# Performance work log

Measured on AMD Instinct MI355X. Metric: run time of the kernel, lower is better.

Reference implementation:

```python
import jax, jax.numpy as jnp
import numpy as np

N_HEAD = 16


def setup_inputs() -> dict:
    key = jax.random.key(0)
    ks = jax.random.split(key, 6)
    B, T, C = 2, 2048, 1024
    x = jax.random.normal(ks[0], (B, T, C), dtype=jnp.float32)
    mask = jnp.ones((B, T), dtype=jnp.int32)
    s = 1.0 / np.sqrt(C)
    Wqkv = jax.random.normal(ks[1], (C, 3 * C), dtype=jnp.float32) * s
    bqkv = jax.random.normal(ks[2], (3 * C,), dtype=jnp.float32) * 0.02
    Wproj = jax.random.normal(ks[3], (C, C), dtype=jnp.float32) * s
    bproj = jax.random.normal(ks[4], (C,), dtype=jnp.float32) * 0.02
    return {"x": x, "mask": mask, "Wqkv": Wqkv, "bqkv": bqkv,
            "Wproj": Wproj, "bproj": bproj}


def reference(x, mask, Wqkv, bqkv, Wproj, bproj):
    B, T, C = x.shape
    H = N_HEAD
    Dh = C // H
    scale = 1.0 / np.sqrt(Dh)
    qkv = x @ Wqkv + bqkv                       # [B,T,3C]
    q, k, v = jnp.split(qkv, 3, axis=-1)
    # [B,T,C] -> [B,H,T,Dh]
    q = q.reshape(B, T, H, Dh).transpose(0, 2, 1, 3)
    k = k.reshape(B, T, H, Dh).transpose(0, 2, 1, 3)
    v = v.reshape(B, T, H, Dh).transpose(0, 2, 1, 3)
    attn = jnp.einsum('bhid,bhjd->bhij', q, k) * scale  # [B,H,T,T]
    m = mask[:, None, None, :]                  # b j -> b 1 1 j
    attn = jnp.where(m == 0, -jnp.inf, attn)
    attn = jax.nn.softmax(attn, axis=-1)
    y = jnp.einsum('bhij,bhjd->bhid', attn, v)  # [B,H,T,Dh]
    y = y.transpose(0, 2, 1, 3).reshape(B, T, C)
    return y @ Wproj + bproj
```

## Files before the change

### kernel.cpp

```cpp
#include <hip/hip_runtime.h>

using US   = unsigned short;
using bf8  = __attribute__((ext_vector_type(8))) __bf16;
using us8  = __attribute__((ext_vector_type(8))) US;
using us4  = __attribute__((ext_vector_type(4))) US;
using f4   = __attribute__((ext_vector_type(4))) float;
using f8   = __attribute__((ext_vector_type(8))) float;
using f16v = __attribute__((ext_vector_type(16))) float;
using i4   = __attribute__((ext_vector_type(4))) int;
using u2   = __attribute__((ext_vector_type(2))) unsigned;

__device__ __forceinline__ US f2bf(float x) {
  union { float f; unsigned u; } v; v.f = x;
  unsigned r = v.u + 0x7fffu + ((v.u >> 16) & 1u);
  return (US)(r >> 16);
}
__device__ __forceinline__ unsigned cvtpk(float a, float b) {
  unsigned r;
  asm("v_cvt_pk_bf16_f32 %0, %1, %2" : "=v"(r) : "v"(a), "v"(b));
  return r;
}
#if __has_builtin(__builtin_amdgcn_exp2f)
__device__ __forceinline__ float ex2(float x) { return __builtin_amdgcn_exp2f(x); }
#else
__device__ __forceinline__ float ex2(float x) {
  float r;
  asm("v_exp_f32 %0, %1" : "=v"(r) : "v"(x));
  return r;
}
#endif
__device__ __forceinline__ void gl16(const US* g, US* l) {
  __builtin_amdgcn_global_load_lds((const __attribute__((address_space(1))) void*)g,
                                   (__attribute__((address_space(3))) void*)l, 16, 0, 0);
}

__global__ void prep_k(const float* __restrict__ x, US* __restrict__ xb,
                       const float* __restrict__ Wqkv, US* __restrict__ WqkvT,
                       const float* __restrict__ Wproj, US* __restrict__ WprojT) {
  __shared__ float tile[32][33];
  int bid = blockIdx.x;
  if (bid < 2048) {
    int i = bid * 256 + threadIdx.x;
    f8 v = ((const f8*)x)[i];
    us8 o;
#pragma unroll
    for (int j = 0; j < 8; ++j) o[j] = f2bf(v[j]);
    ((us8*)xb)[i] = o;
    return;
  }
  const float* in;
  US* out;
  int R, C, tx0, ty0;
  if (bid < 2048 + 3072) {
    int tid = bid - 2048;
    in = Wqkv; out = WqkvT; R = 1024; C = 3072;
    tx0 = (tid % 96) * 32; ty0 = (tid / 96) * 32;
  } else {
    int tid = bid - 2048 - 3072;
    in = Wproj; out = WprojT; R = 1024; C = 1024;
    tx0 = (tid % 32) * 32; ty0 = (tid / 32) * 32;
  }
  int tx = threadIdx.x & 31, ty = threadIdx.x >> 5;
  for (int i = ty; i < 32; i += 8)
    tile[i][tx] = in[(size_t)(ty0 + i) * C + tx0 + tx];
  __syncthreads();
  for (int i = ty; i < 32; i += 8)
    out[(size_t)(tx0 + i) * R + ty0 + tx] = f2bf(tile[tx][i]);
}

__device__ __forceinline__ int SW4(int row) { return (row & 3) ^ ((row >> 2) & 3); }

template <typename OT, bool QSC = false, bool VT = false, int NREP = 4>
__global__ __launch_bounds__(256, 2) void gemm_ct(const US* __restrict__ A,
                                                  const US* __restrict__ Bt,
                                                  const float* __restrict__ bias,
                                                  OT* __restrict__ out,
                                                  US* __restrict__ vtout,
                                                  int M, int N, int K) {
  __shared__ US lA[3][128 * 32];
  __shared__ US lB[3][NREP * 32 * 32];
  const int t = threadIdx.x;
  const int lane = t & 63;
  const int w = t >> 6;
  const int wr = w >> 1, wc = w & 1;
  const int l15 = lane & 15, g = lane >> 4;
  const int id = blockIdx.x;
  const int xcd = id & 7;
  const int s = id >> 3;
  const int m0 = (xcd * 4 + (s & 3)) * 128;
  const int n0 = (s >> 2) * (NREP * 32);

  float bv[NREP];
#pragma unroll
  for (int ni = 0; ni < NREP; ++ni)
    bv[ni] = bias ? bias[n0 + wc * (NREP * 16) + ni * 16 + l15] : 0.0f;

  const int r16 = lane >> 2;
  const int u4 = lane & 3;
  const int csw = (u4 ^ SW4(r16)) * 8;

#define GSTAGE(buf, k0s)                                                          \
  {                                                                               \
    _Pragma("unroll") for (int ss = 0; ss < 2; ++ss) {                            \
      const int rb = w * 32 + ss * 16;                                            \
      gl16(A + (size_t)(m0 + rb + r16) * K + (k0s) + csw, &lA[buf][rb * 32]);     \
    }                                                                             \
    _Pragma("unroll") for (int ss = 0; ss < NREP / 2; ++ss) {                     \
      const int rb = w * (8 * NREP) + ss * 16;                                    \
      gl16(Bt + (size_t)(n0 + rb + r16) * K + (k0s) + csw, &lB[buf][rb * 32]);    \
    }                                                                             \
  }

  GSTAGE(0, 0);

  f4 acc[4][NREP] = {};

#define GTILE(tt, CUR, NXT, LAST)                                              \
  {                                                                            \
    if (!(LAST)) {                                                             \
      GSTAGE(NXT, ((tt) + 1) * 32);                                            \
      if constexpr (NREP == 4)                                                 \
        asm volatile("s_waitcnt vmcnt(4)" ::: "memory");                       \
      else                                                                     \
        asm volatile("s_waitcnt vmcnt(3)" ::: "memory");                       \
    } else {                                                                   \
      asm volatile("s_waitcnt vmcnt(0)" ::: "memory");                         \
    }                                                                          \
    __builtin_amdgcn_s_barrier();                                              \
    asm volatile("" ::: "memory");                                             \
    const US* a_ = lA[CUR];                                                    \
    const US* b_ = lB[CUR];                                                    \
    bf8 af[4], bfr[NREP];                                                      \
    _Pragma("unroll") for (int mi = 0; mi < 4; ++mi) {                         \
      int row = wr * 64 + mi * 16 + l15;                                       \
      af[mi] = *(const bf8*)((const char*)a_ + row * 64 + ((g ^ SW4(row)) << 4)); \
    }                                                                          \
    _Pragma("unroll") for (int ni = 0; ni < NREP; ++ni) {                      \
      int row = wc * (NREP * 16) + ni * 16 + l15;                              \
      bfr[ni] = *(const bf8*)((const char*)b_ + row * 64 + ((g ^ SW4(row)) << 4)); \
    }                                                                          \
    __builtin_amdgcn_s_setprio(1);                                             \
    _Pragma("unroll") for (int mi = 0; mi < 4; ++mi)                           \
      _Pragma("unroll") for (int ni = 0; ni < NREP; ++ni)                      \
        acc[mi][ni] = __builtin_amdgcn_mfma_f32_16x16x32_bf16(af[mi], bfr[ni], acc[mi][ni], 0, 0, 0); \
    __builtin_amdgcn_s_setprio(0);                                             \
  }

  for (int gg = 0; gg < 10; ++gg) {
    const int t3 = gg * 3;
    GTILE(t3, 0, 1, 0)
    GTILE(t3 + 1, 1, 2, 0)
    GTILE(t3 + 2, 2, 0, 0)
  }
  GTILE(30, 0, 1, 0)
  GTILE(31, 1, 2, 1)
#undef GTILE
#undef GSTAGE

  if constexpr (VT) {
    if (n0 >= 2048) {
#pragma unroll
      for (int ni = 0; ni < NREP; ++ni) {
        int cv = n0 - 2048 + wc * (NREP * 16) + ni * 16 + l15;
        int h2 = cv >> 6, d = cv & 63;
#pragma unroll
        for (int mi = 0; mi < 4; ++mi) {
          int rowb = m0 + wr * 64 + mi * 16 + g * 4;
          int bb = rowb >> 11, tloc = rowb & 2047;
          us4 pk;
#pragma unroll
          for (int r = 0; r < 4; ++r) pk[r] = f2bf(acc[mi][ni][r] + bv[ni]);
          *(us4*)(vtout + ((size_t)(bb * 16 + h2) * 64 + d) * 2048 + tloc) = pk;
        }
      }
      return;
    }
  }
  const float oscale = (QSC && n0 < 1024) ? 0.18033688011f : 1.0f;
#pragma unroll
  for (int ni = 0; ni < NREP; ++ni) {
    int col = n0 + wc * (NREP * 16) + ni * 16 + l15;
#pragma unroll
    for (int mi = 0; mi < 4; ++mi) {
      int rowb = m0 + wr * 64 + mi * 16 + g * 4;
#pragma unroll
      for (int r = 0; r < 4; ++r) {
        float val = (acc[mi][ni][r] + bv[ni]) * oscale;
        if constexpr (sizeof(OT) == 2)
          out[(size_t)(rowb + r) * N + col] = f2bf(val);
        else
          out[(size_t)(rowb + r) * N + col] = val;
      }
    }
  }
}

__device__ __forceinline__ const bf8* fragp(const US* base, int r, int ks, int hi) {
  int byte = r * 128 + ((((ks << 1) | hi) ^ (r & 7)) << 4);
  return (const bf8*)((const char*)base + byte);
}

__global__ __launch_bounds__(256, 2) void attn_k(const US* __restrict__ qkv,
                                                 const US* __restrict__ vt,
                                                 const int* __restrict__ mask,
                                                 US* __restrict__ y) {
  int f0 = blockIdx.x;
  int f = ((f0 & 7) << 6) | (f0 >> 3);
  const int qt = f & 15;
  const int bh = f >> 4;
  const int b = bh >> 4;
  const int h = bh & 15;
  const int lane = threadIdx.x & 63, w = threadIdx.x >> 6;
  const int l31 = lane & 31, hi = lane >> 5;

  __shared__ US lK[4][64 * 64];
  __shared__ US lV[4][64 * 64];
  __shared__ unsigned char lMaskB[256];

  const int qr0 = qt * 128 + w * 32;
  const US* qrow = qkv + (size_t)(b * 2048 + qr0 + l31) * 3072 + h * 64 + hi * 8;
  bf8 qf[4];
#pragma unroll
  for (int ks = 0; ks < 4; ++ks) qf[ks] = *(const bf8*)(qrow + ks * 16);

  const int r8 = lane >> 3;
  const int c16 = (lane & 7) ^ r8;
  const US* kg = qkv + (size_t)b * 2048 * 3072 + 1024 + h * 64 + c16 * 8;
  const US* vg = vt + (size_t)bh * 64 * 2048 + c16 * 8;
  const int R0 = w * 16;

  f16v o0 = {}, o1 = {};
  f16v osum = {};
  bf8 pf[4] = {};
  bf8 ones;
  {
    union { US u[8]; bf8 v; } on;
#pragma unroll
    for (int i = 0; i < 8; ++i) on.u[i] = 0x3F80;
    ones = on.v;
  }

#define STAGE(buf, j0s)                                                        \
  {                                                                            \
    gl16(kg + (size_t)((j0s) + R0 + r8) * 3072, &lK[buf][R0 * 64]);            \
    gl16(kg + (size_t)((j0s) + R0 + 8 + r8) * 3072, &lK[buf][(R0 + 8) * 64]);  \
    gl16(vg + (size_t)(R0 + r8) * 2048 + (j0s), &lV[buf][R0 * 64]);            \
    gl16(vg + (size_t)(R0 + 8 + r8) * 2048 + (j0s), &lV[buf][(R0 + 8) * 64]);  \
  }

  STAGE(0, 0);

  int allones;
  {
    const int t8 = threadIdx.x * 8;
    i4 ma = *(const i4*)(mask + b * 2048 + t8);
    i4 mc = *(const i4*)(mask + b * 2048 + t8 + 4);
    unsigned byte = 0;
#pragma unroll
    for (int k = 0; k < 4; ++k) {
      byte |= (ma[k] != 0 ? 1u : 0u) << k;
      byte |= (mc[k] != 0 ? 1u : 0u) << (k + 4);
    }
    lMaskB[threadIdx.x] = (unsigned char)byte;
    allones = __syncthreads_and((int)(byte == 0xFFu));
  }

#pragma unroll 4
  for (int tt = 0; tt < 32; ++tt) {
    const int cur = tt & 3;
    const int j0 = tt * 64;
    if (tt < 31) {
      STAGE((tt + 1) & 3, j0 + 64);
      asm volatile("s_waitcnt vmcnt(4)" ::: "memory");
    } else {
      asm volatile("s_waitcnt vmcnt(0)" ::: "memory");
    }
    __builtin_amdgcn_s_barrier();
    asm volatile("" ::: "memory");

    const US* lKc = lK[cur];

    f16v s0 = {}, s1 = {};
    __builtin_amdgcn_s_setprio(1);
#pragma unroll
    for (int ks = 0; ks < 4; ++ks) {
      bf8 ka0 = *fragp(lKc, l31, ks, hi);
      bf8 ka1 = *fragp(lKc, 32 + l31, ks, hi);
      s0 = __builtin_amdgcn_mfma_f32_32x32x16_bf16(ka0, qf[ks], s0, 0, 0, 0);
      s1 = __builtin_amdgcn_mfma_f32_32x32x16_bf16(ka1, qf[ks], s1, 0, 0, 0);
    }
    if (tt) {
      const US* lVp = lV[(tt + 3) & 3];
#pragma unroll
      for (int ks = 0; ks < 4; ++ks) {
        bf8 vf0 = *fragp(lVp, l31, ks, hi);
        bf8 vf1 = *fragp(lVp, 32 + l31, ks, hi);
        o0 = __builtin_amdgcn_mfma_f32_32x32x16_bf16(vf0, pf[ks], o0, 0, 0, 0);
        o1 = __builtin_amdgcn_mfma_f32_32x32x16_bf16(vf1, pf[ks], o1, 0, 0, 0);
        osum = __builtin_amdgcn_mfma_f32_32x32x16_bf16(ones, pf[ks], osum, 0, 0, 0);
      }
    }
    __builtin_amdgcn_s_setprio(0);

#pragma unroll
    for (int i = 0; i < 16; ++i) {
      s0[i] = ex2(s0[i]);
      s1[i] = ex2(s1[i]);
    }
    if (!allones) {
      unsigned mbyte = lMaskB[(j0 >> 3) + (lane >> 3)];
      int mword = (mbyte >> (lane & 7)) & 1;
      unsigned long long mbits = __ballot(mword != 0);
#pragma unroll
      for (int i = 0; i < 16; ++i) {
        int r = (i & 3) + 8 * (i >> 2) + 4 * hi;
        if (!((mbits >> r) & 1)) s0[i] = 0.0f;
        if (!((mbits >> (32 + r)) & 1)) s1[i] = 0.0f;
      }
    }

#pragma unroll
    for (int ks = 0; ks < 4; ++ks) {
      const f16v& st = (ks < 2) ? s0 : s1;
      const int R = (ks & 1) * 8;
      unsigned w0 = cvtpk(st[R + 0], st[R + 1]);
      unsigned w1 = cvtpk(st[R + 2], st[R + 3]);
      unsigned w2 = cvtpk(st[R + 4], st[R + 5]);
      unsigned w3 = cvtpk(st[R + 6], st[R + 7]);
      u2 p02 = __builtin_amdgcn_permlane32_swap(w0, w2, false, false);
      u2 p13 = __builtin_amdgcn_permlane32_swap(w1, w3, false, false);
      union { unsigned u[4]; bf8 v; } bld;
      bld.u[0] = p02[0];
      bld.u[1] = p13[0];
      bld.u[2] = p02[1];
      bld.u[3] = p13[1];
      pf[ks] = bld.v;
    }
  }
#undef STAGE

  {
    const US* lVp = lV[3];
    __builtin_amdgcn_s_setprio(1);
#pragma unroll
    for (int ks = 0; ks < 4; ++ks) {
      bf8 vf0 = *fragp(lVp, l31, ks, hi);
      bf8 vf1 = *fragp(lVp, 32 + l31, ks, hi);
      o0 = __builtin_amdgcn_mfma_f32_32x32x16_bf16(vf0, pf[ks], o0, 0, 0, 0);
      o1 = __builtin_amdgcn_mfma_f32_32x32x16_bf16(vf1, pf[ks], o1, 0, 0, 0);
      osum = __builtin_amdgcn_mfma_f32_32x32x16_bf16(ones, pf[ks], osum, 0, 0, 0);
    }
    __builtin_amdgcn_s_setprio(0);
  }

  float inv = 1.0f / osum[0];
  US* yrow = y + (size_t)(b * 2048 + qr0 + l31) * 1024 + h * 64;
#pragma unroll
  for (int qd = 0; qd < 4; ++qd) {
    us4 pk0, pk1;
#pragma unroll
    for (int j = 0; j < 4; ++j) {
      pk0[j] = f2bf(o0[qd * 4 + j] * inv);
      pk1[j] = f2bf(o1[qd * 4 + j] * inv);
    }
    *(us4*)(yrow + qd * 8 + hi * 4) = pk0;
    *(us4*)(yrow + 32 + qd * 8 + hi * 4) = pk1;
  }
}

extern "C" void kernel_launch(void* const* d_in, const int* in_sizes, int n_in,
                              void* d_out, int out_size, void* d_ws, size_t ws_size,
                              hipStream_t stream) {
  const float* x     = (const float*)d_in[0];
  const int*   mask  = (const int*)d_in[1];
  const float* Wqkv  = (const float*)d_in[2];
  const float* bqkv  = (const float*)d_in[3];
  const float* Wproj = (const float*)d_in[4];
  const float* bproj = (const float*)d_in[5];
  float* out = (float*)d_out;

  US* xb     = (US*)d_ws;
  US* qkvb   = xb     + (size_t)4096 * 1024;
  US* WqkvT  = qkvb   + (size_t)4096 * 3072;
  US* WprojT = WqkvT  + (size_t)3072 * 1024;
  US* Vt     = WprojT + (size_t)1024 * 1024;
  US* yb     = Vt     + (size_t)32 * 64 * 2048;

  prep_k<<<6144, 256, 0, stream>>>(x, xb, Wqkv, WqkvT, Wproj, WprojT);
  gemm_ct<US, true, true, 4><<<768, 256, 0, stream>>>(xb, WqkvT, bqkv, qkvb, Vt, 4096, 3072, 1024);
  attn_k<<<512, 256, 0, stream>>>(qkvb, Vt, mask, yb);
  gemm_ct<float, false, false, 2><<<512, 256, 0, stream>>>(yb, WprojT, bproj, out, nullptr, 4096, 1024, 1024);
}
```

Before: 107.4 us.

## Use a larger 256x128-tile, 512-thread GEMM for the QKV projection

Adds a new gemm_big kernel that computes the QKV projection with 256x128 output tiles and 8 waves per block, using a triple-buffered LDS pipeline and the same Q scaling and V-transpose epilogue. The launch drops from 768 to 384 blocks. Larger tiles raise operand reuse per LDS load and per global fetch. In exchange, the grid is now roughly 1.5 blocks per CU on 256 CUs, so wave quantization and occupancy may suffer, and LDS use per block grows.

```diff
diff --git a/kernel.cpp b/kernel.cpp
--- a/kernel.cpp
+++ b/kernel.cpp
@@ -69,6 +69,120 @@
 }
 
 __device__ __forceinline__ int SW4(int row) { return (row & 3) ^ ((row >> 2) & 3); }
+
+__global__ __launch_bounds__(512, 4) void gemm_big(const US* __restrict__ A,
+                                                   const US* __restrict__ Bt,
+                                                   const float* __restrict__ bias,
+                                                   US* __restrict__ out,
+                                                   US* __restrict__ vtout,
+                                                   int M, int N, int K) {
+  __shared__ US lA[3][256 * 32];
+  __shared__ US lB[3][128 * 32];
+  const int t = threadIdx.x;
+  const int lane = t & 63;
+  const int w = t >> 6;
+  const int wr = w >> 1, wc = w & 1;
+  const int l15 = lane & 15, g = lane >> 4;
+  const int id = blockIdx.x;
+  const int xcd = id & 7;
+  const int s = id >> 3;
+  const int m0 = (xcd * 2 + (s & 1)) * 256;
+  const int n0 = (s >> 1) * 128;
+
+  float bv[4];
+#pragma unroll
+  for (int ni = 0; ni < 4; ++ni)
+    bv[ni] = bias ? bias[n0 + wc * 64 + ni * 16 + l15] : 0.0f;
+
+  const int r16 = lane >> 2;
+  const int u4 = lane & 3;
+  const int csw = (u4 ^ SW4(r16)) * 8;
+
+#define BSTAGE(buf, k0s)                                                          \
+  {                                                                               \
+    _Pragma("unroll") for (int ss = 0; ss < 2; ++ss) {                            \
+      const int rb = w * 32 + ss * 16;                                            \
+      gl16(A + (size_t)(m0 + rb + r16) * K + (k0s) + csw, &lA[buf][rb * 32]);     \
+    }                                                                             \
+    {                                                                             \
+      const int rb = w * 16;                                                      \
+      gl16(Bt + (size_t)(n0 + rb + r16) * K + (k0s) + csw, &lB[buf][rb * 32]);    \
+    }                                                                             \
+  }
+
+  BSTAGE(0, 0);
+
+  f4 acc[4][4] = {};
+
+#define BTILE(tt, CUR, NXT, LAST)                                              \
+  {                                                                            \
+    if (!(LAST)) {                                                             \
+      BSTAGE(NXT, ((tt) + 1) * 32);                                            \
+      asm volatile("s_waitcnt vmcnt(3)" ::: "memory");                         \
+    } else {                                                                   \
+      asm volatile("s_waitcnt vmcnt(0)" ::: "memory");                         \
+    }                                                                          \
+    __builtin_amdgcn_s_barrier();                                              \
+    asm volatile("" ::: "memory");                                             \
+    const US* a_ = lA[CUR];                                                    \
+    const US* b_ = lB[CUR];                                                    \
+    bf8 af[4], bfr[4];                                                         \
+    _Pragma("unroll") for (int mi = 0; mi < 4; ++mi) {                         \
+      int row = wr * 64 + mi * 16 + l15;                                       \
+      af[mi] = *(const bf8*)((const char*)a_ + row * 64 + ((g ^ SW4(row)) << 4)); \
+    }                                                                          \
+    _Pragma("unroll") for (int ni = 0; ni < 4; ++ni) {                         \
+      int row = wc * 64 + ni * 16 + l15;                                       \
+      bfr[ni] = *(const bf8*)((const char*)b_ + row * 64 + ((g ^ SW4(row)) << 4)); \
+    }                                                                          \
+    __builtin_amdgcn_s_setprio(1);                                             \
+    _Pragma("unroll") for (int mi = 0; mi < 4; ++mi)                           \
+      _Pragma("unroll") for (int ni = 0; ni < 4; ++ni)                         \
+        acc[mi][ni] = __builtin_amdgcn_mfma_f32_16x16x32_bf16(af[mi], bfr[ni], acc[mi][ni], 0, 0, 0); \
+    __builtin_amdgcn_s_setprio(0);                                             \
+  }
+
+  for (int gg = 0; gg < 10; ++gg) {
+    const int t3 = gg * 3;
+    BTILE(t3, 0, 1, 0)
+    BTILE(t3 + 1, 1, 2, 0)
+    BTILE(t3 + 2, 2, 0, 0)
+  }
+  BTILE(30, 0, 1, 0)
+  BTILE(31, 1, 2, 1)
+#undef BTILE
+#undef BSTAGE
+
+  if (n0 >= 2048) {
+#pragma unroll
+    for (int ni = 0; ni < 4; ++ni) {
+      int cv = n0 - 2048 + wc * 64 + ni * 16 + l15;
+      int h2 = cv >> 6, d = cv & 63;
+#pragma unroll
+      for (int mi = 0; mi < 4; ++mi) {
+        int rowb = m0 + wr * 64 + mi * 16 + g * 4;
+        int bb = rowb >> 11, tloc = rowb & 2047;
+        us4 pk;
+#pragma unroll
+        for (int r = 0; r < 4; ++r) pk[r] = f2bf(acc[mi][ni][r] + bv[ni]);
+        *(us4*)(vtout + ((size_t)(bb * 16 + h2) * 64 + d) * 2048 + tloc) = pk;
+      }
+    }
+    return;
+  }
+  const float oscale = (n0 < 1024) ? 0.18033688011f : 1.0f;
+#pragma unroll
+  for (int ni = 0; ni < 4; ++ni) {
+    int col = n0 + wc * 64 + ni * 16 + l15;
+#pragma unroll
+    for (int mi = 0; mi < 4; ++mi) {
+      int rowb = m0 + wr * 64 + mi * 16 + g * 4;
+#pragma unroll
+      for (int r = 0; r < 4; ++r)
+        out[(size_t)(rowb + r) * N + col] = f2bf((acc[mi][ni][r] + bv[ni]) * oscale);
+    }
+  }
+}
 
 template <typename OT, bool QSC = false, bool VT = false, int NREP = 4>
 __global__ __launch_bounds__(256, 2) void gemm_ct(const US* __restrict__ A,
@@ -387,7 +501,7 @@
   US* yb     = Vt     + (size_t)32 * 64 * 2048;
 
   prep_k<<<6144, 256, 0, stream>>>(x, xb, Wqkv, WqkvT, Wproj, WprojT);
-  gemm_ct<US, true, true, 4><<<768, 256, 0, stream>>>(xb, WqkvT, bqkv, qkvb, Vt, 4096, 3072, 1024);
+  gemm_big<<<384, 512, 0, stream>>>(xb, WqkvT, bqkv, qkvb, Vt, 4096, 3072, 1024);
   attn_k<<<512, 256, 0, stream>>>(qkvb, Vt, mask, yb);
   gemm_ct<float, false, false, 2><<<512, 256, 0, stream>>>(yb, WprojT, bproj, out, nullptr, 4096, 1024, 1024);
 }
```

Measured after the change: 109.2 us. No clear change (+1.6%).
